# Kernel optimization log

Measured on AMD Instinct MI355X. Metric: run time of the kernel, lower is better.

## Reference

```python
import jax, jax.numpy as jnp
import numpy as np

KERNEL_SIZE = 5
EPS = 1e-4


def _sliding_sum(a, k, axis):
    cs = jnp.cumsum(a, axis=axis)
    zshape = list(a.shape)
    zshape[axis] = 1
    cs = jnp.concatenate([jnp.zeros(zshape, a.dtype), cs], axis=axis)
    n = cs.shape[axis]
    hi = jax.lax.slice_in_dim(cs, k, n, axis=axis)
    lo = jax.lax.slice_in_dim(cs, 0, n - k, axis=axis)
    return hi - lo


def box_blur(x, k):
    # x: [B, C, H, W]; normalized box filter with reflect padding (matches kornia box_blur)
    p = k // 2
    xp = jnp.pad(x, ((0, 0), (0, 0), (p, p), (p, p)), mode='reflect')
    s = _sliding_sum(_sliding_sum(xp, k, 2), k, 3)
    return s / jnp.asarray(k * k, x.dtype)


def guided_blur_multichannel(guidance, inp, k, eps):
    B, C, H, W = guidance.shape
    Cp = inp.shape[1]

    mean_I = box_blur(guidance, k)                                   # [B,C,H,W]
    corr_I = box_blur((guidance[:, None] * guidance[:, :, None]).reshape(B, C * C, H, W), k)
    var_I = corr_I.reshape(B, C, C, H, W) - mean_I[:, None] * mean_I[:, :, None]

    mean_p = box_blur(inp, k)                                        # [B,Cp,H,W]
    corr_Ip = box_blur((inp[:, None] * guidance[:, :, None]).reshape(B, C * Cp, H, W), k)
    cov_Ip = corr_Ip.reshape(B, C, Cp, H, W) - mean_p[:, None] * mean_I[:, :, None]

    eye = jnp.eye(C, dtype=guidance.dtype).reshape(1, C, C, 1, 1) * eps
    A = jnp.transpose(var_I + eye, (0, 3, 4, 1, 2))                  # [B,H,W,C,C]
    rhs = jnp.transpose(cov_Ip, (0, 3, 4, 1, 2))                     # [B,H,W,C,Cp]
    a = jnp.linalg.solve(A, rhs)                                     # [B,H,W,C,Cp]

    mean_I_hw = jnp.transpose(mean_I, (0, 2, 3, 1))                  # [B,H,W,C]
    mean_p_hw = jnp.transpose(mean_p, (0, 2, 3, 1))                  # [B,H,W,Cp]
    b = mean_p_hw - jnp.einsum('bhwcp,bhwc->bhwp', a, mean_I_hw)     # [B,H,W,Cp]

    a_ch = jnp.transpose(a.reshape(B, H, W, C * Cp), (0, 3, 1, 2))   # [B,C*Cp,H,W]
    b_ch = jnp.transpose(b, (0, 3, 1, 2))                            # [B,Cp,H,W]
    mean_a = jnp.transpose(box_blur(a_ch, k), (0, 2, 3, 1)).reshape(B, H, W, C, Cp)
    mean_b = box_blur(b_ch, k)                                       # [B,Cp,H,W]

    g_hw = jnp.transpose(guidance, (0, 2, 3, 1))                     # [B,H,W,C]
    out_hw = jnp.einsum('bhwc,bhwcp->bhwp', g_hw, mean_a)            # [B,H,W,Cp]
    return jnp.transpose(out_hw, (0, 3, 1, 2)) + mean_b              # [B,Cp,H,W]


def setup_inputs() -> dict:
    key = jax.random.key(0)
    k1, k2 = jax.random.split(key)
    guidance = jax.random.uniform(k1, (8, 3, 512, 512), dtype=jnp.float32)
    inp = jax.random.uniform(k2, (8, 3, 512, 512), dtype=jnp.float32)
    return {"guidance": guidance, "input": inp}


def reference(guidance, input):
    return guided_blur_multichannel(guidance, input, KERNEL_SIZE, EPS)
```

## Files before the change

### kernel.cpp

```cpp
#include <hip/hip_runtime.h>


namespace {

constexpr int BN = 8;
constexpr int HH = 512;
constexpr int WW = 512;
constexpr int CSZ = HH * WW;
constexpr float GEPS = 1e-4f;
constexpr int SEGW = 8;
constexpr int OUTW = 4 * SEGW;
constexpr int SR   = 32;

__device__ __forceinline__ int refl(int i, int n) {
    if (i < 0) i = -i;
    if (i >= n) i = 2 * n - 2 - i;
    return i;
}

template <int N>
__device__ __forceinline__ float shlN(float v) {
    return __builtin_bit_cast(float,
        __builtin_amdgcn_update_dpp(0, __builtin_bit_cast(int, v),
                                    0x100 + N, 0xF, 0xF, true));
}
__device__ __forceinline__ float hsum5(float v) {
    float t = v + shlN<1>(v);
    float q = t + shlN<2>(t);
    return q + shlN<4>(v);
}

struct St {
    float P[6];
    float V1[21];
    float r1[5][6];
    float V2[12];
    float r2[5][12];
};

struct Ctx {
    const float *g0, *g1, *g2, *p0, *p1, *p2;
    float *o0, *o1, *o2;
    int yb, xr, xs;
    bool wr;
};

template <int I, bool SUB1, bool SOLVE, bool V2SUB, bool OUT, bool PF>
__device__ __forceinline__ void row(St& st, const Ctx& cx, int t) {
    const int rr = 5 * t + I;

    float c0 = st.P[0], c1 = st.P[1], c2 = st.P[2];
    float c3 = st.P[3], c4 = st.P[4], c5 = st.P[5];

    if constexpr (PF) {
        const int yn = refl(cx.yb - 4 + rr + 1, HH);
        const int offn = yn * WW + cx.xr;
        st.P[0] = cx.g0[offn]; st.P[1] = cx.g1[offn]; st.P[2] = cx.g2[offn];
        st.P[3] = cx.p0[offn]; st.P[4] = cx.p1[offn]; st.P[5] = cx.p2[offn];
    }

    st.V1[0] += c0; st.V1[1] += c1; st.V1[2] += c2;
    st.V1[3] += c3; st.V1[4] += c4; st.V1[5] += c5;
    st.V1[6]  += c0 * c0; st.V1[7]  += c0 * c1; st.V1[8]  += c0 * c2;
    st.V1[9]  += c1 * c1; st.V1[10] += c1 * c2; st.V1[11] += c2 * c2;
    st.V1[12] += c0 * c3; st.V1[13] += c0 * c4; st.V1[14] += c0 * c5;
    st.V1[15] += c1 * c3; st.V1[16] += c1 * c4; st.V1[17] += c1 * c5;
    st.V1[18] += c2 * c3; st.V1[19] += c2 * c4; st.V1[20] += c2 * c5;

    if constexpr (SUB1) {
        float o0 = st.r1[I][0], o1 = st.r1[I][1], o2 = st.r1[I][2];
        float o3 = st.r1[I][3], o4 = st.r1[I][4], o5 = st.r1[I][5];
        st.V1[0] -= o0; st.V1[1] -= o1; st.V1[2] -= o2;
        st.V1[3] -= o3; st.V1[4] -= o4; st.V1[5] -= o5;
        st.V1[6]  -= o0 * o0; st.V1[7]  -= o0 * o1; st.V1[8]  -= o0 * o2;
        st.V1[9]  -= o1 * o1; st.V1[10] -= o1 * o2; st.V1[11] -= o2 * o2;
        st.V1[12] -= o0 * o3; st.V1[13] -= o0 * o4; st.V1[14] -= o0 * o5;
        st.V1[15] -= o1 * o3; st.V1[16] -= o1 * o4; st.V1[17] -= o1 * o5;
        st.V1[18] -= o2 * o3; st.V1[19] -= o2 * o4; st.V1[20] -= o2 * o5;
    }
    st.r1[I][0] = c0; st.r1[I][1] = c1; st.r1[I][2] = c2;
    st.r1[I][3] = c3; st.r1[I][4] = c4; st.r1[I][5] = c5;

    if constexpr (SOLVE) {
        float S[21];
#pragma unroll
        for (int c = 0; c < 21; ++c) S[c] = hsum5(st.V1[c]);

        const float nrm = 0.04f;
        float mI0 = S[0] * nrm, mI1 = S[1] * nrm, mI2 = S[2] * nrm;
        float mP0 = S[3] * nrm, mP1 = S[4] * nrm, mP2 = S[5] * nrm;
        float v00 = S[6]  * nrm - mI0 * mI0 + GEPS;
        float v01 = S[7]  * nrm - mI0 * mI1;
        float v02 = S[8]  * nrm - mI0 * mI2;
        float v11 = S[9]  * nrm - mI1 * mI1 + GEPS;
        float v12 = S[10] * nrm - mI1 * mI2;
        float v22 = S[11] * nrm - mI2 * mI2 + GEPS;
        float c00 = S[12] * nrm - mI0 * mP0;
        float c01 = S[13] * nrm - mI0 * mP1;
        float c02 = S[14] * nrm - mI0 * mP2;
        float c10 = S[15] * nrm - mI1 * mP0;
        float c11 = S[16] * nrm - mI1 * mP1;
        float c12 = S[17] * nrm - mI1 * mP2;
        float c20 = S[18] * nrm - mI2 * mP0;
        float c21 = S[19] * nrm - mI2 * mP1;
        float c22 = S[20] * nrm - mI2 * mP2;
        float i00 = v11 * v22 - v12 * v12;
        float i01 = v02 * v12 - v01 * v22;
        float i02 = v01 * v12 - v02 * v11;
        float i11 = v00 * v22 - v02 * v02;
        float i12 = v01 * v02 - v00 * v12;
        float i22 = v00 * v11 - v01 * v01;
        float det = v00 * i00 + v01 * i01 + v02 * i02;
        float rd  = __builtin_amdgcn_rcpf(det);
        float a00 = (i00 * c00 + i01 * c10 + i02 * c20) * rd;
        float a01 = (i00 * c01 + i01 * c11 + i02 * c21) * rd;
        float a02 = (i00 * c02 + i01 * c12 + i02 * c22) * rd;
        float a10 = (i01 * c00 + i11 * c10 + i12 * c20) * rd;
        float a11 = (i01 * c01 + i11 * c11 + i12 * c21) * rd;
        float a12 = (i01 * c02 + i11 * c12 + i12 * c22) * rd;
        float a20 = (i02 * c00 + i12 * c10 + i22 * c20) * rd;
        float a21 = (i02 * c01 + i12 * c11 + i22 * c21) * rd;
        float a22 = (i02 * c02 + i12 * c12 + i22 * c22) * rd;
        float b0 = mP0 - (a00 * mI0 + a10 * mI1 + a20 * mI2);
        float b1 = mP1 - (a01 * mI0 + a11 * mI1 + a21 * mI2);
        float b2 = mP2 - (a02 * mI0 + a12 * mI1 + a22 * mI2);

        float hv[12];
        hv[0] = hsum5(a00); hv[1]  = hsum5(a01); hv[2]  = hsum5(a02);
        hv[3] = hsum5(a10); hv[4]  = hsum5(a11); hv[5]  = hsum5(a12);
        hv[6] = hsum5(a20); hv[7]  = hsum5(a21); hv[8]  = hsum5(a22);
        hv[9] = hsum5(b0);  hv[10] = hsum5(b1);  hv[11] = hsum5(b2);

#pragma unroll
        for (int c = 0; c < 12; ++c) {
            st.V2[c] += hv[c];
            if constexpr (V2SUB) st.V2[c] -= st.r2[I][c];
            st.r2[I][c] = hv[c];
        }

        if constexpr (OUT) {
            constexpr int J = (I + 1) % 5;
            float gg0 = shlN<4>(st.r1[J][0]);
            float gg1 = shlN<4>(st.r1[J][1]);
            float gg2 = shlN<4>(st.r1[J][2]);
            const int oOff = (cx.yb + rr - 8) * WW + cx.xs;
            float M[12];
#pragma unroll
            for (int c = 0; c < 12; ++c) M[c] = st.V2[c] * 0.04f;
            float o0 = gg0 * M[0] + gg1 * M[3] + gg2 * M[6] + M[9];
            float o1 = gg0 * M[1] + gg1 * M[4] + gg2 * M[7] + M[10];
            float o2 = gg0 * M[2] + gg1 * M[5] + gg2 * M[8] + M[11];
            if (cx.wr) {
                cx.o0[oOff] = o0;
                cx.o1[oOff] = o1;
                cx.o2[oOff] = o2;
            }
        }
    }
}

__global__ __launch_bounds__(64, 2) void fused_kernel(
        const float* __restrict__ g, const float* __restrict__ p,
        float* __restrict__ out) {
    const int lane = threadIdx.x;
    const int l    = lane & 15;
    const int seg  = lane >> 4;
    const int XO   = blockIdx.x * OUTW;
    const int bb   = blockIdx.z;

    const int xbase = XO + seg * SEGW - 2;
    const int xrq   = xbase + l - 2;
    const int xo    = xbase + l + 2;

    Ctx cx;
    cx.g0 = g + (size_t)bb * 3 * CSZ; cx.g1 = cx.g0 + CSZ; cx.g2 = cx.g0 + 2 * CSZ;
    cx.p0 = p + (size_t)bb * 3 * CSZ; cx.p1 = cx.p0 + CSZ; cx.p2 = cx.p0 + 2 * CSZ;
    cx.o0 = out + (size_t)bb * 3 * CSZ; cx.o1 = cx.o0 + CSZ; cx.o2 = cx.o0 + 2 * CSZ;
    cx.yb = blockIdx.y * SR;
    cx.xr = refl(xrq, WW);
    cx.xs = (xo < WW) ? xo : (WW - 1);
    cx.wr = (l < SEGW);

    St st;
#pragma unroll
    for (int i = 0; i < 21; ++i) st.V1[i] = 0.f;
#pragma unroll
    for (int i = 0; i < 12; ++i) st.V2[i] = 0.f;

    {
        const int y0 = refl(cx.yb - 4, HH);
        const int off0 = y0 * WW + cx.xr;
        st.P[0] = cx.g0[off0]; st.P[1] = cx.g1[off0]; st.P[2] = cx.g2[off0];
        st.P[3] = cx.p0[off0]; st.P[4] = cx.p1[off0]; st.P[5] = cx.p2[off0];
    }

    row<0, false, false, false, false, true>(st, cx, 0);
    row<1, false, false, false, false, true>(st, cx, 0);
    row<2, false, false, false, false, true>(st, cx, 0);
    row<3, false, false, false, false, true>(st, cx, 0);
    row<4, false, true,  false, false, true>(st, cx, 0);
    row<0, true, true, false, false, true>(st, cx, 1);
    row<1, true, true, false, false, true>(st, cx, 1);
    row<2, true, true, false, false, true>(st, cx, 1);
    row<3, true, true, false, true,  true>(st, cx, 1);
    row<4, true, true, true,  true,  true>(st, cx, 1);
#pragma unroll 1
    for (int t = 2; t <= 6; ++t) {
        row<0, true, true, true, true, true>(st, cx, t);
        row<1, true, true, true, true, true>(st, cx, t);
        row<2, true, true, true, true, true>(st, cx, t);
        row<3, true, true, true, true, true>(st, cx, t);
        row<4, true, true, true, true, true>(st, cx, t);
    }
    row<0, true, true, true, true, true >(st, cx, 7);
    row<1, true, true, true, true, true >(st, cx, 7);
    row<2, true, true, true, true, true >(st, cx, 7);
    row<3, true, true, true, true, true >(st, cx, 7);
    row<4, true, true, true, true, false>(st, cx, 7);
}

}

extern "C" void kernel_launch(void* const* d_in, const int* in_sizes, int n_in,
                              void* d_out, int out_size, void* d_ws, size_t ws_size,
                              hipStream_t stream) {
    const float* g  = (const float*)d_in[0];
    const float* p  = (const float*)d_in[1];
    float* out = (float*)d_out;

    dim3 grid(WW / OUTW, HH / SR, BN);
    dim3 block(64);

    hipLaunchKernelGGL(fused_kernel, grid, block, 0, stream, g, p, out);
}
```

Measured before the change: 130.2 us.

## Use full-wave column tiles with bpermute shifts and deeper row prefetch

Replaces the four 16-lane segments (8 useful output columns each) with one 64-lane strip producing 56 output columns per wave, which cuts the redundant halo loads and recomputation between segments. Because the horizontal shifts now have to cross 16-lane rows, the DPP row shifts are replaced with ds_bpermute, which goes through LDS hardware and has higher latency. The row prefetch buffer grows from one row to five rows, so global loads are issued further ahead of use at the cost of more registers. The grid shrinks to 10 blocks across x, with the last block masking its out-of-range columns.

Result: slower. 150.8 us (+15.8%).

```diff
diff --git a/kernel.cpp b/kernel.cpp
--- a/kernel.cpp
+++ b/kernel.cpp
@@ -8,8 +8,8 @@
 constexpr int WW = 512;
 constexpr int CSZ = HH * WW;
 constexpr float GEPS = 1e-4f;
-constexpr int SEGW = 8;
-constexpr int OUTW = 4 * SEGW;
+constexpr int OUTW = 56;
+constexpr int XBLK = 10;
 constexpr int SR   = 32;
 
 __device__ __forceinline__ int refl(int i, int n) {
@@ -18,45 +18,45 @@
     return i;
 }
 
-template <int N>
-__device__ __forceinline__ float shlN(float v) {
+__device__ __forceinline__ float shl_b(int idxB, float v) {
     return __builtin_bit_cast(float,
-        __builtin_amdgcn_update_dpp(0, __builtin_bit_cast(int, v),
-                                    0x100 + N, 0xF, 0xF, true));
-}
-__device__ __forceinline__ float hsum5(float v) {
-    float t = v + shlN<1>(v);
-    float q = t + shlN<2>(t);
-    return q + shlN<4>(v);
+        __builtin_amdgcn_ds_bpermute(idxB, __builtin_bit_cast(int, v)));
+}
+
+struct Ctx {
+    const float *g0, *g1, *g2, *p0, *p1, *p2;
+    float *o0, *o1, *o2;
+    int yb, xr, xo;
+    int i1, i2, i4;
+    bool wr;
+};
+
+__device__ __forceinline__ float hsum5(const Ctx& cx, float v) {
+    float t = v + shl_b(cx.i1, v);
+    float q = t + shl_b(cx.i2, t);
+    return q + shl_b(cx.i4, v);
 }
 
 struct St {
-    float P[6];
+    float P[5][6];
     float V1[21];
     float r1[5][6];
     float V2[12];
     float r2[5][12];
 };
 
-struct Ctx {
-    const float *g0, *g1, *g2, *p0, *p1, *p2;
-    float *o0, *o1, *o2;
-    int yb, xr, xs;
-    bool wr;
-};
-
 template <int I, bool SUB1, bool SOLVE, bool V2SUB, bool OUT, bool PF>
 __device__ __forceinline__ void row(St& st, const Ctx& cx, int t) {
     const int rr = 5 * t + I;
 
-    float c0 = st.P[0], c1 = st.P[1], c2 = st.P[2];
-    float c3 = st.P[3], c4 = st.P[4], c5 = st.P[5];
+    float c0 = st.P[I][0], c1 = st.P[I][1], c2 = st.P[I][2];
+    float c3 = st.P[I][3], c4 = st.P[I][4], c5 = st.P[I][5];
 
     if constexpr (PF) {
-        const int yn = refl(cx.yb - 4 + rr + 1, HH);
+        const int yn = refl(cx.yb - 4 + rr + 5, HH);
         const int offn = yn * WW + cx.xr;
-        st.P[0] = cx.g0[offn]; st.P[1] = cx.g1[offn]; st.P[2] = cx.g2[offn];
-        st.P[3] = cx.p0[offn]; st.P[4] = cx.p1[offn]; st.P[5] = cx.p2[offn];
+        st.P[I][0] = cx.g0[offn]; st.P[I][1] = cx.g1[offn]; st.P[I][2] = cx.g2[offn];
+        st.P[I][3] = cx.p0[offn]; st.P[I][4] = cx.p1[offn]; st.P[I][5] = cx.p2[offn];
     }
 
     st.V1[0] += c0; st.V1[1] += c1; st.V1[2] += c2;
@@ -84,7 +84,7 @@
     if constexpr (SOLVE) {
         float S[21];
 #pragma unroll
-        for (int c = 0; c < 21; ++c) S[c] = hsum5(st.V1[c]);
+        for (int c = 0; c < 21; ++c) S[c] = hsum5(cx, st.V1[c]);
 
         const float nrm = 0.04f;
         float mI0 = S[0] * nrm, mI1 = S[1] * nrm, mI2 = S[2] * nrm;
@@ -126,10 +126,10 @@
         float b2 = mP2 - (a02 * mI0 + a12 * mI1 + a22 * mI2);
 
         float hv[12];
-        hv[0] = hsum5(a00); hv[1]  = hsum5(a01); hv[2]  = hsum5(a02);
-        hv[3] = hsum5(a10); hv[4]  = hsum5(a11); hv[5]  = hsum5(a12);
-        hv[6] = hsum5(a20); hv[7]  = hsum5(a21); hv[8]  = hsum5(a22);
-        hv[9] = hsum5(b0);  hv[10] = hsum5(b1);  hv[11] = hsum5(b2);
+        hv[0] = hsum5(cx, a00); hv[1]  = hsum5(cx, a01); hv[2]  = hsum5(cx, a02);
+        hv[3] = hsum5(cx, a10); hv[4]  = hsum5(cx, a11); hv[5]  = hsum5(cx, a12);
+        hv[6] = hsum5(cx, a20); hv[7]  = hsum5(cx, a21); hv[8]  = hsum5(cx, a22);
+        hv[9] = hsum5(cx, b0);  hv[10] = hsum5(cx, b1);  hv[11] = hsum5(cx, b2);
 
 #pragma unroll
         for (int c = 0; c < 12; ++c) {
@@ -140,10 +140,10 @@
 
         if constexpr (OUT) {
             constexpr int J = (I + 1) % 5;
-            float gg0 = shlN<4>(st.r1[J][0]);
-            float gg1 = shlN<4>(st.r1[J][1]);
-            float gg2 = shlN<4>(st.r1[J][2]);
-            const int oOff = (cx.yb + rr - 8) * WW + cx.xs;
+            float gg0 = shl_b(cx.i4, st.r1[J][0]);
+            float gg1 = shl_b(cx.i4, st.r1[J][1]);
+            float gg2 = shl_b(cx.i4, st.r1[J][2]);
+            const int oOff = (cx.yb + rr - 8) * WW + cx.xo;
             float M[12];
 #pragma unroll
             for (int c = 0; c < 12; ++c) M[c] = st.V2[c] * 0.04f;
@@ -163,23 +163,22 @@
         const float* __restrict__ g, const float* __restrict__ p,
         float* __restrict__ out) {
     const int lane = threadIdx.x;
-    const int l    = lane & 15;
-    const int seg  = lane >> 4;
-    const int XO   = blockIdx.x * OUTW;
     const int bb   = blockIdx.z;
-
-    const int xbase = XO + seg * SEGW - 2;
-    const int xrq   = xbase + l - 2;
-    const int xo    = xbase + l + 2;
+    const int xob  = blockIdx.x * OUTW;
+
+    const int xq = xob - 4 + lane;
 
     Ctx cx;
     cx.g0 = g + (size_t)bb * 3 * CSZ; cx.g1 = cx.g0 + CSZ; cx.g2 = cx.g0 + 2 * CSZ;
     cx.p0 = p + (size_t)bb * 3 * CSZ; cx.p1 = cx.p0 + CSZ; cx.p2 = cx.p0 + 2 * CSZ;
     cx.o0 = out + (size_t)bb * 3 * CSZ; cx.o1 = cx.o0 + CSZ; cx.o2 = cx.o0 + 2 * CSZ;
     cx.yb = blockIdx.y * SR;
-    cx.xr = refl(xrq, WW);
-    cx.xs = (xo < WW) ? xo : (WW - 1);
-    cx.wr = (l < SEGW);
+    cx.xr = refl(xq, WW);
+    cx.xo = xob + lane;
+    cx.wr = (lane < OUTW) && (cx.xo < WW);
+    cx.i1 = (lane + 1) << 2;
+    cx.i2 = (lane + 2) << 2;
+    cx.i4 = (lane + 4) << 2;
 
     St st;
 #pragma unroll
@@ -187,11 +186,12 @@
 #pragma unroll
     for (int i = 0; i < 12; ++i) st.V2[i] = 0.f;
 
-    {
-        const int y0 = refl(cx.yb - 4, HH);
+#pragma unroll
+    for (int j = 0; j < 5; ++j) {
+        const int y0 = refl(cx.yb - 4 + j, HH);
         const int off0 = y0 * WW + cx.xr;
-        st.P[0] = cx.g0[off0]; st.P[1] = cx.g1[off0]; st.P[2] = cx.g2[off0];
-        st.P[3] = cx.p0[off0]; st.P[4] = cx.p1[off0]; st.P[5] = cx.p2[off0];
+        st.P[j][0] = cx.g0[off0]; st.P[j][1] = cx.g1[off0]; st.P[j][2] = cx.g2[off0];
+        st.P[j][3] = cx.p0[off0]; st.P[j][4] = cx.p1[off0]; st.P[j][5] = cx.p2[off0];
     }
 
     row<0, false, false, false, false, true>(st, cx, 0);
@@ -212,10 +212,10 @@
         row<3, true, true, true, true, true>(st, cx, t);
         row<4, true, true, true, true, true>(st, cx, t);
     }
-    row<0, true, true, true, true, true >(st, cx, 7);
-    row<1, true, true, true, true, true >(st, cx, 7);
-    row<2, true, true, true, true, true >(st, cx, 7);
-    row<3, true, true, true, true, true >(st, cx, 7);
+    row<0, true, true, true, true, false>(st, cx, 7);
+    row<1, true, true, true, true, false>(st, cx, 7);
+    row<2, true, true, true, true, false>(st, cx, 7);
+    row<3, true, true, true, true, false>(st, cx, 7);
     row<4, true, true, true, true, false>(st, cx, 7);
 }
 
@@ -228,7 +228,7 @@
     const float* p  = (const float*)d_in[1];
     float* out = (float*)d_out;
 
-    dim3 grid(WW / OUTW, HH / SR, BN);
+    dim3 grid(XBLK, HH / SR, BN);
     dim3 block(64);
 
     hipLaunchKernelGGL(fused_kernel, grid, block, 0, stream, g, p, out);
```

## Software-pipeline solve and second blur stage across rows

Applied to the files above, without the earlier changes.

Splits the per-row work into a first stage (vertical accumulation, 3x3 solve producing a/b coefficients) and a second stage (horizontal sum, vertical accumulation of coefficients, output). The second stage for the previous row now runs before the first stage of the current row, so the solve result is carried across iterations in registers. This gives the scheduler independent work to interleave and hides DPP and ALU latency chains, at the cost of 12 more live registers and an extra epilogue row with shifted output indexing. The prefetch on the final row is also no longer disabled.

Result: no change. 132.1 us (+1.4%).

```diff
diff --git a/kernel.cpp b/kernel.cpp
--- a/kernel.cpp
+++ b/kernel.cpp
@@ -36,6 +36,7 @@
     float r1[5][6];
     float V2[12];
     float r2[5][12];
+    float A[12];
 };
 
 struct Ctx {
@@ -45,10 +46,42 @@
     bool wr;
 };
 
-template <int I, bool SUB1, bool SOLVE, bool V2SUB, bool OUT, bool PF>
-__device__ __forceinline__ void row(St& st, const Ctx& cx, int t) {
-    const int rr = 5 * t + I;
-
+template <int I, bool V2SUB, bool OUT>
+__device__ __forceinline__ void stage2(St& st, const Ctx& cx, int rr) {
+    float hv[12];
+    hv[0] = hsum5(st.A[0]); hv[1]  = hsum5(st.A[1]); hv[2]  = hsum5(st.A[2]);
+    hv[3] = hsum5(st.A[3]); hv[4]  = hsum5(st.A[4]); hv[5]  = hsum5(st.A[5]);
+    hv[6] = hsum5(st.A[6]); hv[7]  = hsum5(st.A[7]); hv[8]  = hsum5(st.A[8]);
+    hv[9] = hsum5(st.A[9]); hv[10] = hsum5(st.A[10]); hv[11] = hsum5(st.A[11]);
+
+#pragma unroll
+    for (int c = 0; c < 12; ++c) {
+        st.V2[c] += hv[c];
+        if constexpr (V2SUB) st.V2[c] -= st.r2[I][c];
+        st.r2[I][c] = hv[c];
+    }
+
+    if constexpr (OUT) {
+        float gg0 = shlN<4>(st.r1[I][0]);
+        float gg1 = shlN<4>(st.r1[I][1]);
+        float gg2 = shlN<4>(st.r1[I][2]);
+        const int oOff = (cx.yb + rr - 9) * WW + cx.xs;
+        float M[12];
+#pragma unroll
+        for (int c = 0; c < 12; ++c) M[c] = st.V2[c] * 0.04f;
+        float o0 = gg0 * M[0] + gg1 * M[3] + gg2 * M[6] + M[9];
+        float o1 = gg0 * M[1] + gg1 * M[4] + gg2 * M[7] + M[10];
+        float o2 = gg0 * M[2] + gg1 * M[5] + gg2 * M[8] + M[11];
+        if (cx.wr) {
+            cx.o0[oOff] = o0;
+            cx.o1[oOff] = o1;
+            cx.o2[oOff] = o2;
+        }
+    }
+}
+
+template <int I, bool SUB1, bool SOLVE, bool PF>
+__device__ __forceinline__ void stage1(St& st, const Ctx& cx, int rr) {
     float c0 = st.P[0], c1 = st.P[1], c2 = st.P[2];
     float c3 = st.P[3], c4 = st.P[4], c5 = st.P[5];
 
@@ -112,50 +145,18 @@
         float i22 = v00 * v11 - v01 * v01;
         float det = v00 * i00 + v01 * i01 + v02 * i02;
         float rd  = __builtin_amdgcn_rcpf(det);
-        float a00 = (i00 * c00 + i01 * c10 + i02 * c20) * rd;
-        float a01 = (i00 * c01 + i01 * c11 + i02 * c21) * rd;
-        float a02 = (i00 * c02 + i01 * c12 + i02 * c22) * rd;
-        float a10 = (i01 * c00 + i11 * c10 + i12 * c20) * rd;
-        float a11 = (i01 * c01 + i11 * c11 + i12 * c21) * rd;
-        float a12 = (i01 * c02 + i11 * c12 + i12 * c22) * rd;
-        float a20 = (i02 * c00 + i12 * c10 + i22 * c20) * rd;
-        float a21 = (i02 * c01 + i12 * c11 + i22 * c21) * rd;
-        float a22 = (i02 * c02 + i12 * c12 + i22 * c22) * rd;
-        float b0 = mP0 - (a00 * mI0 + a10 * mI1 + a20 * mI2);
-        float b1 = mP1 - (a01 * mI0 + a11 * mI1 + a21 * mI2);
-        float b2 = mP2 - (a02 * mI0 + a12 * mI1 + a22 * mI2);
-
-        float hv[12];
-        hv[0] = hsum5(a00); hv[1]  = hsum5(a01); hv[2]  = hsum5(a02);
-        hv[3] = hsum5(a10); hv[4]  = hsum5(a11); hv[5]  = hsum5(a12);
-        hv[6] = hsum5(a20); hv[7]  = hsum5(a21); hv[8]  = hsum5(a22);
-        hv[9] = hsum5(b0);  hv[10] = hsum5(b1);  hv[11] = hsum5(b2);
-
-#pragma unroll
-        for (int c = 0; c < 12; ++c) {
-            st.V2[c] += hv[c];
-            if constexpr (V2SUB) st.V2[c] -= st.r2[I][c];
-            st.r2[I][c] = hv[c];
-        }
-
-        if constexpr (OUT) {
-            constexpr int J = (I + 1) % 5;
-            float gg0 = shlN<4>(st.r1[J][0]);
-            float gg1 = shlN<4>(st.r1[J][1]);
-            float gg2 = shlN<4>(st.r1[J][2]);
-            const int oOff = (cx.yb + rr - 8) * WW + cx.xs;
-            float M[12];
-#pragma unroll
-            for (int c = 0; c < 12; ++c) M[c] = st.V2[c] * 0.04f;
-            float o0 = gg0 * M[0] + gg1 * M[3] + gg2 * M[6] + M[9];
-            float o1 = gg0 * M[1] + gg1 * M[4] + gg2 * M[7] + M[10];
-            float o2 = gg0 * M[2] + gg1 * M[5] + gg2 * M[8] + M[11];
-            if (cx.wr) {
-                cx.o0[oOff] = o0;
-                cx.o1[oOff] = o1;
-                cx.o2[oOff] = o2;
-            }
-        }
+        st.A[0]  = (i00 * c00 + i01 * c10 + i02 * c20) * rd;
+        st.A[1]  = (i00 * c01 + i01 * c11 + i02 * c21) * rd;
+        st.A[2]  = (i00 * c02 + i01 * c12 + i02 * c22) * rd;
+        st.A[3]  = (i01 * c00 + i11 * c10 + i12 * c20) * rd;
+        st.A[4]  = (i01 * c01 + i11 * c11 + i12 * c21) * rd;
+        st.A[5]  = (i01 * c02 + i11 * c12 + i12 * c22) * rd;
+        st.A[6]  = (i02 * c00 + i12 * c10 + i22 * c20) * rd;
+        st.A[7]  = (i02 * c01 + i12 * c11 + i22 * c21) * rd;
+        st.A[8]  = (i02 * c02 + i12 * c12 + i22 * c22) * rd;
+        st.A[9]  = mP0 - (st.A[0] * mI0 + st.A[3] * mI1 + st.A[6] * mI2);
+        st.A[10] = mP1 - (st.A[1] * mI0 + st.A[4] * mI1 + st.A[7] * mI2);
+        st.A[11] = mP2 - (st.A[2] * mI0 + st.A[5] * mI1 + st.A[8] * mI2);
     }
 }
 
@@ -194,29 +195,26 @@
         st.P[3] = cx.p0[off0]; st.P[4] = cx.p1[off0]; st.P[5] = cx.p2[off0];
     }
 
-    row<0, false, false, false, false, true>(st, cx, 0);
-    row<1, false, false, false, false, true>(st, cx, 0);
-    row<2, false, false, false, false, true>(st, cx, 0);
-    row<3, false, false, false, false, true>(st, cx, 0);
-    row<4, false, true,  false, false, true>(st, cx, 0);
-    row<0, true, true, false, false, true>(st, cx, 1);
-    row<1, true, true, false, false, true>(st, cx, 1);
-    row<2, true, true, false, false, true>(st, cx, 1);
-    row<3, true, true, false, true,  true>(st, cx, 1);
-    row<4, true, true, true,  true,  true>(st, cx, 1);
+    stage1<0, false, false, true>(st, cx, 0);
+    stage1<1, false, false, true>(st, cx, 1);
+    stage1<2, false, false, true>(st, cx, 2);
+    stage1<3, false, false, true>(st, cx, 3);
+    stage1<4, false, true,  true>(st, cx, 4);
+    stage2<0, false, false>(st, cx, 5); stage1<0, true, true, true>(st, cx, 5);
+    stage2<1, false, false>(st, cx, 6); stage1<1, true, true, true>(st, cx, 6);
+    stage2<2, false, false>(st, cx, 7); stage1<2, true, true, true>(st, cx, 7);
+    stage2<3, false, false>(st, cx, 8); stage1<3, true, true, true>(st, cx, 8);
+    stage2<4, false, true >(st, cx, 9); stage1<4, true, true, true>(st, cx, 9);
 #pragma unroll 1
-    for (int t = 2; t <= 6; ++t) {
-        row<0, true, true, true, true, true>(st, cx, t);
-        row<1, true, true, true, true, true>(st, cx, t);
-        row<2, true, true, true, true, true>(st, cx, t);
-        row<3, true, true, true, true, true>(st, cx, t);
-        row<4, true, true, true, true, true>(st, cx, t);
-    }
-    row<0, true, true, true, true, true >(st, cx, 7);
-    row<1, true, true, true, true, true >(st, cx, 7);
-    row<2, true, true, true, true, true >(st, cx, 7);
-    row<3, true, true, true, true, true >(st, cx, 7);
-    row<4, true, true, true, true, false>(st, cx, 7);
+    for (int t = 2; t <= 7; ++t) {
+        const int rrb = 5 * t;
+        stage2<0, true, true>(st, cx, rrb + 0); stage1<0, true, true, true>(st, cx, rrb + 0);
+        stage2<1, true, true>(st, cx, rrb + 1); stage1<1, true, true, true>(st, cx, rrb + 1);
+        stage2<2, true, true>(st, cx, rrb + 2); stage1<2, true, true, true>(st, cx, rrb + 2);
+        stage2<3, true, true>(st, cx, rrb + 3); stage1<3, true, true, true>(st, cx, rrb + 3);
+        stage2<4, true, true>(st, cx, rrb + 4); stage1<4, true, true, true>(st, cx, rrb + 4);
+    }
+    stage2<0, true, true>(st, cx, 40);
 }
 
 }
```
